# Performance work log

Measured on AMD Instinct MI355X. Metric: run time of the kernel, lower is better.

## Reference

```python
import jax, jax.numpy as jnp
import numpy as np
from jax import lax

N = 512          # batch size
A = 64 * 3 * 3 + 1  # 577 minibatch-disc input features
B = 32           # out_features of minibatch disc
C = 16           # kernel dimension


def leaky_relu(x, slope=0.2):
    return jnp.where(x >= 0, x, slope * x)


def setup_inputs() -> dict:
    key = jax.random.key(0)
    ks = jax.random.split(key, 9)
    readout = jax.random.normal(ks[0], (N, 1, 9, 9), dtype=jnp.float32)
    energy = jax.random.uniform(ks[1], (N,), dtype=jnp.float32)
    conv1_w = jax.random.normal(ks[2], (32, 1, 4, 4), dtype=jnp.float32) * 0.1
    conv2_w = jax.random.normal(ks[3], (64, 32, 4, 4), dtype=jnp.float32) * 0.05
    T = jax.random.normal(ks[4], (A, B * C), dtype=jnp.float32)  # init.normal(0,1)
    W1 = jax.random.normal(ks[5], (32, A + B), dtype=jnp.float32) * 0.04
    b1 = jax.random.normal(ks[6], (32,), dtype=jnp.float32) * 0.01
    W2 = jax.random.normal(ks[7], (1, 32), dtype=jnp.float32) * 0.1
    b2 = jax.random.normal(ks[8], (1,), dtype=jnp.float32) * 0.01
    return {"readout": readout, "energy": energy, "conv1_w": conv1_w,
            "conv2_w": conv2_w, "T": T, "W1": W1, "b1": b1, "W2": W2, "b2": b2}


def _conv(x, w):
    return lax.conv_general_dilated(
        x, w, window_strides=(1, 1), padding='VALID',
        dimension_numbers=('NCHW', 'OIHW', 'NCHW'))


def reference(readout, energy, conv1_w, conv2_w, T, W1, b1, W2, b2):
    n = readout.shape[0]
    # conv stack: (n,1,9,9) -> (n,32,6,6) -> (n,64,3,3)
    h = leaky_relu(_conv(readout, conv1_w))
    h = leaky_relu(_conv(h, conv2_w))
    hidden = h.reshape(n, -1)  # (n, 576)
    reco_energy = readout.reshape(n, -1).sum(axis=1)
    energy_diff = jnp.abs(reco_energy - energy)[:, None]  # (n,1)
    f = jnp.concatenate([hidden, energy_diff], axis=1)  # (n, 577)
    # minibatch discrimination
    M = (f @ T).reshape(n, B, C)                     # (n,B,C)
    # L1 pairwise distances, summed over kernel dim C: (n,n,B)
    L1 = jnp.abs(M[None, :, :, :] - M[:, None, :, :]).sum(axis=3)
    o = jnp.exp(-L1).sum(axis=0)                     # (n,B)
    x = jnp.concatenate([f, o], axis=1)              # (n, 609)
    x = leaky_relu(x @ W1.T + b1)
    x = jax.nn.sigmoid(x @ W2.T + b2)
    return x.squeeze()
```

## Files before the change

kernel.cpp:

```cpp
#include <hip/hip_runtime.h>

#define LRELU(v) ((v) >= 0.f ? (v) : 0.2f*(v))

#define ROROW(P, RB) \
    const float P##0=ro[(RB)+0], P##1=ro[(RB)+1], P##2=ro[(RB)+2], \
        P##3=ro[(RB)+3], P##4=ro[(RB)+4], P##5=ro[(RB)+5], \
        P##6=ro[(RB)+6], P##7=ro[(RB)+7], P##8=ro[(RB)+8];

#define C1X(X0,X1,X2,X3) \
    (wa.x*A##X0 + wa.y*A##X1 + wa.z*A##X2 + wa.w*A##X3 \
   + wb.x*B##X0 + wb.y*B##X1 + wb.z*B##X2 + wb.w*B##X3 \
   + wc.x*C##X0 + wc.y*C##X1 + wc.z*C##X2 + wc.w*C##X3 \
   + wd.x*D##X0 + wd.y*D##X1 + wd.z*D##X2 + wd.w*D##X3)

#define E0 q0.x
#define E1 q0.y
#define E2 q0.z
#define E3 q0.w
#define E4 q1.x
#define E5 q1.y
#define E6 q1.z
#define E7 q1.w
#define E8 q2.x
#define E9 q2.y
#define E10 q2.z
#define E11 q2.w
#define E12 q3.x
#define E13 q3.y
#define E14 q3.z
#define E15 q3.w
#define E16 q4.x
#define E17 q4.y
#define E18 q4.z
#define E19 q4.w
#define E20 q5.x
#define E21 q5.y
#define E22 q5.z
#define E23 q5.w
#define E24 q6.x
#define E25 q6.y
#define E26 q6.z
#define E27 q6.w
#define E28 q7.x
#define E29 q7.y
#define E30 q7.z
#define E31 q7.w
#define E32 q8.x
#define E33 q8.y
#define E34 q8.z
#define E35 q8.w

#define AT(P, A, B, C, D) a##P += w.x*E##A + w.y*E##B + w.z*E##C + w.w*E##D;

#define LD1(RK, K, BASE) { const int fidx_ = t + (K)*256; \
    const int woc_ = fidx_ >> 5, q4_ = fidx_ & 31; \
    RK = ((const float4*)w2)[(oc0 + woc_)*128 + (BASE) + q4_]; }
#define LDALL(BASE) LD1(r0,0,BASE) LD1(r1,1,BASE) LD1(r2,2,BASE) LD1(r3,3,BASE)
#define ST1(RK, K) { const int fidx_ = t + (K)*256; \
    const int woc_ = fidx_ >> 5, q4_ = fidx_ & 31; \
    *((float4*)&w2s[woc_*128 + ((q4_*4) ^ ((woc_ & 7) << 2))]) = RK; }
#define STALL ST1(r0,0) ST1(r1,1) ST1(r2,2) ST1(r3,3)

__global__ __launch_bounds__(256) void convf_kernel(
    const float* __restrict__ readout, const float* __restrict__ energy,
    const float* __restrict__ w1, const float* __restrict__ w2,
    const float* __restrict__ W1, float* __restrict__ f_ws,
    float* __restrict__ W1T)
{
    const int bid = blockIdx.x;
    const int n   = bid >> 1;
    const int och = bid & 1;
    const int oc0 = och << 5;
    const int t = threadIdx.x;
    __shared__ float ro[81];
    __shared__ float h1[1152];
    __shared__ float w2s[4096];
    __shared__ float red[2304];

    if (t < 81) ro[t] = readout[n*81 + t];
    __syncthreads();

    if (och == 0 && t < 64) {
        float v = ro[t];
        if (t < 17) v += ro[t + 64];
        #pragma unroll
        for (int m = 32; m; m >>= 1) v += __shfl_down(v, m);
        if (t == 0) f_ws[n*577 + 576] = fabsf(v - energy[n]);
    }

    if (t < 192) {
        const int oc1 = t & 31, y = t >> 5;
        const float4* wp4 = (const float4*)&w1[oc1*16];
        const float4 wa = wp4[0], wb = wp4[1], wc = wp4[2], wd = wp4[3];
        const int rb0 = y*9;
        ROROW(A, rb0)
        ROROW(B, rb0+9)
        ROROW(C, rb0+18)
        ROROW(D, rb0+27)
        float* hp = &h1[oc1*36 + y*6];
        float v;
        v = C1X(0,1,2,3); hp[0] = LRELU(v);
        v = C1X(1,2,3,4); hp[1] = LRELU(v);
        v = C1X(2,3,4,5); hp[2] = LRELU(v);
        v = C1X(3,4,5,6); hp[3] = LRELU(v);
        v = C1X(4,5,6,7); hp[4] = LRELU(v);
        v = C1X(5,6,7,8); hp[5] = LRELU(v);
    }

    float4 r0, r1, r2, r3;
    LDALL(0)
    __syncthreads();

    const int ich = t >> 5, ocl = t & 31;
    float a0=0.f,a1=0.f,a2=0.f,a3=0.f,a4=0.f,a5=0.f,a6=0.f,a7=0.f,a8=0.f;
    const int wbase = ocl*128;
    const int wswz  = (ocl & 7) << 2;

    for (int chunk = 0; chunk < 4; chunk++) {
        STALL
        __syncthreads();
        if (chunk < 3) { LDALL((chunk+1)*32) }
        {
            const int icw = ich;
            const int ic  = chunk*8 + ich;
            const float4* hp = (const float4*)&h1[ic*36];
            float4 q0=hp[0], q1=hp[1], q2=hp[2], q3=hp[3], q4=hp[4],
                   q5=hp[5], q6=hp[6], q7=hp[7], q8=hp[8];
            { float4 w = *((const float4*)&w2s[wbase + ((icw*16 + 0) ^ wswz)]);
              AT(0, 0,1,2,3)    AT(1, 1,2,3,4)    AT(2, 2,3,4,5)
              AT(3, 6,7,8,9)    AT(4, 7,8,9,10)   AT(5, 8,9,10,11)
              AT(6, 12,13,14,15) AT(7, 13,14,15,16) AT(8, 14,15,16,17) }
            { float4 w = *((const float4*)&w2s[wbase + ((icw*16 + 4) ^ wswz)]);
              AT(0, 6,7,8,9)    AT(1, 7,8,9,10)   AT(2, 8,9,10,11)
              AT(3, 12,13,14,15) AT(4, 13,14,15,16) AT(5, 14,15,16,17)
              AT(6, 18,19,20,21) AT(7, 19,20,21,22) AT(8, 20,21,22,23) }
            { float4 w = *((const float4*)&w2s[wbase + ((icw*16 + 8) ^ wswz)]);
              AT(0, 12,13,14,15) AT(1, 13,14,15,16) AT(2, 14,15,16,17)
              AT(3, 18,19,20,21) AT(4, 19,20,21,22) AT(5, 20,21,22,23)
              AT(6, 24,25,26,27) AT(7, 25,26,27,28) AT(8, 26,27,28,29) }
            { float4 w = *((const float4*)&w2s[wbase + ((icw*16 + 12) ^ wswz)]);
              AT(0, 18,19,20,21) AT(1, 19,20,21,22) AT(2, 20,21,22,23)
              AT(3, 24,25,26,27) AT(4, 25,26,27,28) AT(5, 26,27,28,29)
              AT(6, 30,31,32,33) AT(7, 31,32,33,34) AT(8, 32,33,34,35) }
        }
        __syncthreads();
    }

    {
        float* rp = &red[t*9];
        rp[0]=a0; rp[1]=a1; rp[2]=a2; rp[3]=a3; rp[4]=a4;
        rp[5]=a5; rp[6]=a6; rp[7]=a7; rp[8]=a8;
    }
    __syncthreads();
    for (int idx = t; idx < 288; idx += 256) {
        const int o2 = idx / 9, pos = idx % 9;
        float v = 0.f;
        #pragma unroll
        for (int k = 0; k < 8; k++) v += red[k*288 + idx];
        f_ws[n*577 + (oc0 + o2)*9 + pos] = LRELU(v);
    }

    if (bid < 8) {
        for (int idx = t; idx < 2436; idx += 256) {
            const int g = bid*2436 + idx;
            const int u = g & 31, a = g >> 5;
            W1T[g] = W1[u*609 + a];
        }
    }
}

__global__ __launch_bounds__(1024) void mgemm_kernel(
    const float* __restrict__ F, const float* __restrict__ T,
    float* __restrict__ M)
{
    const int t = threadIdx.x;
    const int rb = blockIdx.x >> 2;
    const int cb = blockIdx.x & 3;
    const int ws = __builtin_amdgcn_readfirstlane(t >> 6);
    const int lane = t & 63;
    const int c0 = cb*128 + lane*2;
    const int k0 = ws*36;
    const int k1 = (ws == 15) ? 577 : (k0 + 36);
    const int r0 = rb*8;
    __shared__ float red[8*1032];

    const float* fbase = F + r0*577;
    float x0=0.f,y0=0.f, x1=0.f,y1=0.f, x2=0.f,y2=0.f, x3=0.f,y3=0.f,
          x4=0.f,y4=0.f, x5=0.f,y5=0.f, x6=0.f,y6=0.f, x7=0.f,y7=0.f;
    #pragma unroll 4
    for (int k = k0; k < k1; ++k) {
        const float2 tv = *(const float2*)&T[k*512 + c0];
        const float* fr = fbase + k;
        const float f0v = fr[0],    f1v = fr[577],  f2v = fr[1154], f3v = fr[1731];
        const float f4v = fr[2308], f5v = fr[2885], f6v = fr[3462], f7v = fr[4039];
        x0 += f0v*tv.x; y0 += f0v*tv.y;
        x1 += f1v*tv.x; y1 += f1v*tv.y;
        x2 += f2v*tv.x; y2 += f2v*tv.y;
        x3 += f3v*tv.x; y3 += f3v*tv.y;
        x4 += f4v*tv.x; y4 += f4v*tv.y;
        x5 += f5v*tv.x; y5 += f5v*tv.y;
        x6 += f6v*tv.x; y6 += f6v*tv.y;
        x7 += f7v*tv.x; y7 += f7v*tv.y;
    }

    const int cl2 = lane*2;
    if (ws < 8) {
        float* rp = &red[ws*1032];
        *(float2*)&rp[0*128 + cl2] = make_float2(x0, y0);
        *(float2*)&rp[1*128 + cl2] = make_float2(x1, y1);
        *(float2*)&rp[2*128 + cl2] = make_float2(x2, y2);
        *(float2*)&rp[3*128 + cl2] = make_float2(x3, y3);
        *(float2*)&rp[4*128 + cl2] = make_float2(x4, y4);
        *(float2*)&rp[5*128 + cl2] = make_float2(x5, y5);
        *(float2*)&rp[6*128 + cl2] = make_float2(x6, y6);
        *(float2*)&rp[7*128 + cl2] = make_float2(x7, y7);
    }
    __syncthreads();
    if (ws >= 8) {
        float* rp = &red[(ws-8)*1032];
        float2 v;
        v = *(float2*)&rp[0*128 + cl2]; v.x += x0; v.y += y0; *(float2*)&rp[0*128 + cl2] = v;
        v = *(float2*)&rp[1*128 + cl2]; v.x += x1; v.y += y1; *(float2*)&rp[1*128 + cl2] = v;
        v = *(float2*)&rp[2*128 + cl2]; v.x += x2; v.y += y2; *(float2*)&rp[2*128 + cl2] = v;
        v = *(float2*)&rp[3*128 + cl2]; v.x += x3; v.y += y3; *(float2*)&rp[3*128 + cl2] = v;
        v = *(float2*)&rp[4*128 + cl2]; v.x += x4; v.y += y4; *(float2*)&rp[4*128 + cl2] = v;
        v = *(float2*)&rp[5*128 + cl2]; v.x += x5; v.y += y5; *(float2*)&rp[5*128 + cl2] = v;
        v = *(float2*)&rp[6*128 + cl2]; v.x += x6; v.y += y6; *(float2*)&rp[6*128 + cl2] = v;
        v = *(float2*)&rp[7*128 + cl2]; v.x += x7; v.y += y7; *(float2*)&rp[7*128 + cl2] = v;
    }
    __syncthreads();
    {
        const int row = t >> 7, col = t & 127;
        const int o = row*128 + col;
        float v = 0.f;
        #pragma unroll
        for (int p = 0; p < 8; p++) v += red[p*1032 + o];
        M[(r0 + row)*512 + cb*128 + col] = v;
    }
}

#define LDM(R0, R1, R2, R3, JOFF) { \
    const float4* p_ = (const float4*)&M[(j0+jl+(JOFF))*512 + b*16]; \
    R0 = p_[0]; R1 = p_[1]; R2 = p_[2]; R3 = p_[3]; }

#define S16(P0, P1, P2, P3) \
  (fabsf(v0.x-P0.x)+fabsf(v0.y-P0.y)+fabsf(v0.z-P0.z)+fabsf(v0.w-P0.w) \
  +fabsf(v1.x-P1.x)+fabsf(v1.y-P1.y)+fabsf(v1.z-P1.z)+fabsf(v1.w-P1.w) \
  +fabsf(v2.x-P2.x)+fabsf(v2.y-P2.y)+fabsf(v2.z-P2.z)+fabsf(v2.w-P2.w) \
  +fabsf(v3.x-P3.x)+fabsf(v3.y-P3.y)+fabsf(v3.z-P3.z)+fabsf(v3.w-P3.w))

__global__ __launch_bounds__(256) void pairwise_kernel(
    const float* __restrict__ M, float* __restrict__ o_part)
{
    const int jt  = blockIdx.x >> 5;
    const int isp = blockIdx.x & 31;
    const int t = threadIdx.x;
    const int b = t & 31, jl = t >> 5;
    const int j0 = jt * 32;
    __shared__ float mi[16*572];

    float4 mA0,mA1,mA2,mA3, mB0,mB1,mB2,mB3, mC0,mC1,mC2,mC3, mD0,mD1,mD2,mD3;
    LDM(mA0,mA1,mA2,mA3, 0)
    LDM(mB0,mB1,mB2,mB3, 8)
    LDM(mC0,mC1,mC2,mC3, 16)
    LDM(mD0,mD1,mD2,mD3, 24)

    const int i0 = isp * 16;
    #pragma unroll
    for (int k = 0; k < 8; k++) {
        const int q = k*256 + t;
        const int r = q >> 7;
        const int x = (q & 127) * 4;
        float4 v = *(const float4*)&M[(i0+r)*512 + x];
        *(float4*)&mi[r*572 + x + ((x>>5)<<2)] = v;
    }
    __syncthreads();

    float acc0 = 0.f, acc1 = 0.f, acc2 = 0.f, acc3 = 0.f;
    const int lbase = b*16 + ((b>>1)<<2);

    #pragma unroll 4
    for (int r = 0; r < 16; r++) {
        const float4* q_ = (const float4*)&mi[r*572 + lbase];
        const float4 v0 = q_[0], v1 = q_[1], v2 = q_[2], v3 = q_[3];
        acc0 += __expf(-(S16(mA0,mA1,mA2,mA3)));
        acc1 += __expf(-(S16(mB0,mB1,mB2,mB3)));
        acc2 += __expf(-(S16(mC0,mC1,mC2,mC3)));
        acc3 += __expf(-(S16(mD0,mD1,mD2,mD3)));
    }
    const int ob = isp*16384 + b;
    o_part[ob + (j0+jl   )*32] = acc0;
    o_part[ob + (j0+jl+8 )*32] = acc1;
    o_part[ob + (j0+jl+16)*32] = acc2;
    o_part[ob + (j0+jl+24)*32] = acc3;
}

__global__ __launch_bounds__(256) void mlp_kernel(
    const float* __restrict__ f, const float* __restrict__ o_part,
    const float* __restrict__ W1T, const float* __restrict__ b1v,
    const float* __restrict__ W2, const float* __restrict__ b2v,
    float* __restrict__ out)
{
    const int j = blockIdx.x;
    const int t = threadIdx.x;
    __shared__ float xs[609];
    __shared__ float red[256];

    for (int a = t; a < 577; a += 256) xs[a] = f[j*577 + a];
    {
        const int bb = t & 31, g = t >> 5;
        float ov = 0.f;
        #pragma unroll
        for (int k = 0; k < 4; k++)
            ov += o_part[(g + 8*k)*16384 + j*32 + bb];
        red[t] = ov;
    }
    __syncthreads();
    if (t < 32) {
        float ov = 0.f;
        #pragma unroll
        for (int g = 0; g < 8; g++) ov += red[t + g*32];
        xs[577 + t] = ov;
    }
    __syncthreads();

    const int u = t & 31, seg = t >> 5;
    float p = 0.f;
    #pragma unroll 4
    for (int a = seg; a < 609; a += 8)
        p += xs[a] * W1T[a*32 + u];
    red[t] = p;
    __syncthreads();

    if (t < 32) {
        float hid = red[t];
        #pragma unroll
        for (int s = 1; s < 8; s++) hid += red[t + s*32];
        hid += b1v[t];
        hid = LRELU(hid);
        float pr = hid * W2[t];
        #pragma unroll
        for (int mk = 16; mk; mk >>= 1) pr += __shfl_xor(pr, mk);
        if (t == 0) out[j] = 1.f / (1.f + __expf(-(pr + b2v[0])));
    }
}

extern "C" void kernel_launch(void* const* d_in, const int* in_sizes, int n_in,
                              void* d_out, int out_size, void* d_ws, size_t ws_size,
                              hipStream_t stream) {
    const float* readout = (const float*)d_in[0];
    const float* energy  = (const float*)d_in[1];
    const float* w1      = (const float*)d_in[2];
    const float* w2      = (const float*)d_in[3];
    const float* Tm      = (const float*)d_in[4];
    const float* W1      = (const float*)d_in[5];
    const float* b1v     = (const float*)d_in[6];
    const float* W2      = (const float*)d_in[7];
    const float* b2v     = (const float*)d_in[8];
    float* out = (float*)d_out;

    char* ws = (char*)d_ws;
    float* f_ws   = (float*)(ws);
    float* M_ws   = (float*)(ws + 512*577*4);
    float* o_ws   = (float*)(ws + 512*577*4 + 512*512*4);
    float* W1T_ws = (float*)(ws + 512*577*4 + 512*512*4 + 32*512*32*4);

    convf_kernel   <<<1024, 256, 0, stream>>>(readout, energy, w1, w2, W1, f_ws, W1T_ws);
    mgemm_kernel   <<<256, 1024, 0, stream>>>(f_ws, Tm, M_ws);
    pairwise_kernel<<<512, 256, 0, stream>>>(M_ws, o_ws);
    mlp_kernel     <<<512, 256, 0, stream>>>(f_ws, o_ws, W1T_ws, b1v, W2, b2v, out);
}
```

Baseline: 45.62 us.

## Restructure conv2 thread mapping with shuffle reduction and split pairwise i-range finer

The conv2 stage now gives each thread two output channels across 16 input-channel lanes. It loads weights in two larger chunks with a new swizzle and reduces partial sums with warp xor-shuffles, which drops the shared-memory reduction buffer and its extra barrier. The pairwise kernel splits the i dimension into 64 slices of 8 rows instead of 32 slices of 16, doubling the grid to raise parallelism. The mlp kernel sums 64 partials instead of 32 and the workspace offset is adjusted to match. The costs are higher register pressure and more partial-sum traffic.

```diff
diff --git a/kernel.cpp b/kernel.cpp
--- a/kernel.cpp
+++ b/kernel.cpp
@@ -50,16 +50,39 @@
 #define E34 q8.z
 #define E35 q8.w
 
-#define AT(P, A, B, C, D) a##P += w.x*E##A + w.y*E##B + w.z*E##C + w.w*E##D;
-
-#define LD1(RK, K, BASE) { const int fidx_ = t + (K)*256; \
-    const int woc_ = fidx_ >> 5, q4_ = fidx_ & 31; \
-    RK = ((const float4*)w2)[(oc0 + woc_)*128 + (BASE) + q4_]; }
-#define LDALL(BASE) LD1(r0,0,BASE) LD1(r1,1,BASE) LD1(r2,2,BASE) LD1(r3,3,BASE)
+#define AZ(P, I, A, B, C, D) P##I += w.x*E##A + w.y*E##B + w.z*E##C + w.w*E##D;
+
+#define KYB0(P) { AZ(P,0, 0,1,2,3)    AZ(P,1, 1,2,3,4)    AZ(P,2, 2,3,4,5) \
+                  AZ(P,3, 6,7,8,9)    AZ(P,4, 7,8,9,10)   AZ(P,5, 8,9,10,11) \
+                  AZ(P,6, 12,13,14,15) AZ(P,7, 13,14,15,16) AZ(P,8, 14,15,16,17) }
+#define KYB1(P) { AZ(P,0, 6,7,8,9)    AZ(P,1, 7,8,9,10)   AZ(P,2, 8,9,10,11) \
+                  AZ(P,3, 12,13,14,15) AZ(P,4, 13,14,15,16) AZ(P,5, 14,15,16,17) \
+                  AZ(P,6, 18,19,20,21) AZ(P,7, 19,20,21,22) AZ(P,8, 20,21,22,23) }
+#define KYB2(P) { AZ(P,0, 12,13,14,15) AZ(P,1, 13,14,15,16) AZ(P,2, 14,15,16,17) \
+                  AZ(P,3, 18,19,20,21) AZ(P,4, 19,20,21,22) AZ(P,5, 20,21,22,23) \
+                  AZ(P,6, 24,25,26,27) AZ(P,7, 25,26,27,28) AZ(P,8, 26,27,28,29) }
+#define KYB3(P) { AZ(P,0, 18,19,20,21) AZ(P,1, 19,20,21,22) AZ(P,2, 20,21,22,23) \
+                  AZ(P,3, 24,25,26,27) AZ(P,4, 25,26,27,28) AZ(P,5, 26,27,28,29) \
+                  AZ(P,6, 30,31,32,33) AZ(P,7, 31,32,33,34) AZ(P,8, 32,33,34,35) }
+
+#define RED18(M) \
+    a0+=__shfl_xor(a0,M); a1+=__shfl_xor(a1,M); a2+=__shfl_xor(a2,M); \
+    a3+=__shfl_xor(a3,M); a4+=__shfl_xor(a4,M); a5+=__shfl_xor(a5,M); \
+    a6+=__shfl_xor(a6,M); a7+=__shfl_xor(a7,M); a8+=__shfl_xor(a8,M); \
+    g0+=__shfl_xor(g0,M); g1+=__shfl_xor(g1,M); g2+=__shfl_xor(g2,M); \
+    g3+=__shfl_xor(g3,M); g4+=__shfl_xor(g4,M); g5+=__shfl_xor(g5,M); \
+    g6+=__shfl_xor(g6,M); g7+=__shfl_xor(g7,M); g8+=__shfl_xor(g8,M);
+
+#define LD1(RK, K, CH) { const int fidx_ = t + (K)*256; \
+    const int woc_ = fidx_ >> 6, q4_ = fidx_ & 63; \
+    RK = ((const float4*)w2)[(oc0 + woc_)*128 + (CH)*64 + q4_]; }
+#define LDALL(CH) LD1(r0,0,CH) LD1(r1,1,CH) LD1(r2,2,CH) LD1(r3,3,CH) \
+                  LD1(r4,4,CH) LD1(r5,5,CH) LD1(r6,6,CH) LD1(r7,7,CH)
 #define ST1(RK, K) { const int fidx_ = t + (K)*256; \
-    const int woc_ = fidx_ >> 5, q4_ = fidx_ & 31; \
-    *((float4*)&w2s[woc_*128 + ((q4_*4) ^ ((woc_ & 7) << 2))]) = RK; }
-#define STALL ST1(r0,0) ST1(r1,1) ST1(r2,2) ST1(r3,3)
+    const int woc_ = fidx_ >> 6, q4_ = fidx_ & 63; \
+    *((float4*)&w2s[woc_*256 + ((q4_*4) ^ (((woc_>>1)&3)<<3))]) = RK; }
+#define STALL ST1(r0,0) ST1(r1,1) ST1(r2,2) ST1(r3,3) \
+              ST1(r4,4) ST1(r5,5) ST1(r6,6) ST1(r7,7)
 
 __global__ __launch_bounds__(256) void convf_kernel(
     const float* __restrict__ readout, const float* __restrict__ energy,
@@ -74,8 +97,7 @@
     const int t = threadIdx.x;
     __shared__ float ro[81];
     __shared__ float h1[1152];
-    __shared__ float w2s[4096];
-    __shared__ float red[2304];
+    __shared__ float w2s[8192];
 
     if (t < 81) ro[t] = readout[n*81 + t];
     __syncthreads();
@@ -107,57 +129,51 @@
         v = C1X(5,6,7,8); hp[5] = LRELU(v);
     }
 
-    float4 r0, r1, r2, r3;
+    float4 r0, r1, r2, r3, r4, r5, r6, r7;
     LDALL(0)
     __syncthreads();
 
-    const int ich = t >> 5, ocl = t & 31;
+    const int ocp = t >> 4, ich = t & 15;
+    const int ocaL = ocp*2, ocbL = ocaL + 1;
+    const int wswz = (ocp & 3) << 3;
+    const int wbA = ocaL*256, wbB = ocbL*256;
     float a0=0.f,a1=0.f,a2=0.f,a3=0.f,a4=0.f,a5=0.f,a6=0.f,a7=0.f,a8=0.f;
-    const int wbase = ocl*128;
-    const int wswz  = (ocl & 7) << 2;
-
-    for (int chunk = 0; chunk < 4; chunk++) {
+    float g0=0.f,g1=0.f,g2=0.f,g3=0.f,g4=0.f,g5=0.f,g6=0.f,g7=0.f,g8=0.f;
+
+    #pragma unroll 1
+    for (int chunk = 0; chunk < 2; chunk++) {
         STALL
         __syncthreads();
-        if (chunk < 3) { LDALL((chunk+1)*32) }
-        {
-            const int icw = ich;
-            const int ic  = chunk*8 + ich;
-            const float4* hp = (const float4*)&h1[ic*36];
-            float4 q0=hp[0], q1=hp[1], q2=hp[2], q3=hp[3], q4=hp[4],
-                   q5=hp[5], q6=hp[6], q7=hp[7], q8=hp[8];
-            { float4 w = *((const float4*)&w2s[wbase + ((icw*16 + 0) ^ wswz)]);
-              AT(0, 0,1,2,3)    AT(1, 1,2,3,4)    AT(2, 2,3,4,5)
-              AT(3, 6,7,8,9)    AT(4, 7,8,9,10)   AT(5, 8,9,10,11)
-              AT(6, 12,13,14,15) AT(7, 13,14,15,16) AT(8, 14,15,16,17) }
-            { float4 w = *((const float4*)&w2s[wbase + ((icw*16 + 4) ^ wswz)]);
-              AT(0, 6,7,8,9)    AT(1, 7,8,9,10)   AT(2, 8,9,10,11)
-              AT(3, 12,13,14,15) AT(4, 13,14,15,16) AT(5, 14,15,16,17)
-              AT(6, 18,19,20,21) AT(7, 19,20,21,22) AT(8, 20,21,22,23) }
-            { float4 w = *((const float4*)&w2s[wbase + ((icw*16 + 8) ^ wswz)]);
-              AT(0, 12,13,14,15) AT(1, 13,14,15,16) AT(2, 14,15,16,17)
-              AT(3, 18,19,20,21) AT(4, 19,20,21,22) AT(5, 20,21,22,23)
-              AT(6, 24,25,26,27) AT(7, 25,26,27,28) AT(8, 26,27,28,29) }
-            { float4 w = *((const float4*)&w2s[wbase + ((icw*16 + 12) ^ wswz)]);
-              AT(0, 18,19,20,21) AT(1, 19,20,21,22) AT(2, 20,21,22,23)
-              AT(3, 24,25,26,27) AT(4, 25,26,27,28) AT(5, 26,27,28,29)
-              AT(6, 30,31,32,33) AT(7, 31,32,33,34) AT(8, 32,33,34,35) }
-        }
+        if (chunk == 0) { LDALL(1) }
+
+        const int ic = chunk*16 + ich;
+        const float4* hp = (const float4*)&h1[ic*36];
+        const float4 q0=hp[0], q1=hp[1], q2=hp[2], q3=hp[3], q4=hp[4],
+                     q5=hp[5], q6=hp[6], q7=hp[7], q8=hp[8];
+        const int colb = ich*16;
+        { float4 w = *((const float4*)&w2s[wbA + ((colb+ 0) ^ wswz)]); KYB0(a) }
+        { float4 w = *((const float4*)&w2s[wbA + ((colb+ 4) ^ wswz)]); KYB1(a) }
+        { float4 w = *((const float4*)&w2s[wbA + ((colb+ 8) ^ wswz)]); KYB2(a) }
+        { float4 w = *((const float4*)&w2s[wbA + ((colb+12) ^ wswz)]); KYB3(a) }
+        { float4 w = *((const float4*)&w2s[wbB + ((colb+ 0) ^ wswz)]); KYB0(g) }
+        { float4 w = *((const float4*)&w2s[wbB + ((colb+ 4) ^ wswz)]); KYB1(g) }
+        { float4 w = *((const float4*)&w2s[wbB + ((colb+ 8) ^ wswz)]); KYB2(g) }
+        { float4 w = *((const float4*)&w2s[wbB + ((colb+12) ^ wswz)]); KYB3(g) }
         __syncthreads();
     }
 
-    {
-        float* rp = &red[t*9];
-        rp[0]=a0; rp[1]=a1; rp[2]=a2; rp[3]=a3; rp[4]=a4;
-        rp[5]=a5; rp[6]=a6; rp[7]=a7; rp[8]=a8;
-    }
-    __syncthreads();
-    for (int idx = t; idx < 288; idx += 256) {
-        const int o2 = idx / 9, pos = idx % 9;
-        float v = 0.f;
-        #pragma unroll
-        for (int k = 0; k < 8; k++) v += red[k*288 + idx];
-        f_ws[n*577 + (oc0 + o2)*9 + pos] = LRELU(v);
+    RED18(1) RED18(2) RED18(4) RED18(8)
+
+    if (ich == 0) {
+        float* fa = &f_ws[n*577 + (oc0 + ocaL)*9];
+        float* fb = &f_ws[n*577 + (oc0 + ocbL)*9];
+        float v;
+        v=a0; fa[0]=LRELU(v); v=a1; fa[1]=LRELU(v); v=a2; fa[2]=LRELU(v);
+        v=a3; fa[3]=LRELU(v); v=a4; fa[4]=LRELU(v); v=a5; fa[5]=LRELU(v);
+        v=a6; fa[6]=LRELU(v); v=a7; fa[7]=LRELU(v); v=a8; fa[8]=LRELU(v);
+        v=g0; fb[0]=LRELU(v); v=g1; fb[1]=LRELU(v); v=g2; fb[2]=LRELU(v);
+        v=g3; fb[3]=LRELU(v); v=g4; fb[4]=LRELU(v); v=g5; fb[5]=LRELU(v);
+        v=g6; fb[6]=LRELU(v); v=g7; fb[7]=LRELU(v); v=g8; fb[8]=LRELU(v);
     }
 
     if (bid < 8) {
@@ -252,12 +268,12 @@
 __global__ __launch_bounds__(256) void pairwise_kernel(
     const float* __restrict__ M, float* __restrict__ o_part)
 {
-    const int jt  = blockIdx.x >> 5;
-    const int isp = blockIdx.x & 31;
+    const int jt  = blockIdx.x >> 6;
+    const int isp = blockIdx.x & 63;
     const int t = threadIdx.x;
     const int b = t & 31, jl = t >> 5;
     const int j0 = jt * 32;
-    __shared__ float mi[16*572];
+    __shared__ float mi[8*572];
 
     float4 mA0,mA1,mA2,mA3, mB0,mB1,mB2,mB3, mC0,mC1,mC2,mC3, mD0,mD1,mD2,mD3;
     LDM(mA0,mA1,mA2,mA3, 0)
@@ -265,9 +281,9 @@
     LDM(mC0,mC1,mC2,mC3, 16)
     LDM(mD0,mD1,mD2,mD3, 24)
 
-    const int i0 = isp * 16;
+    const int i0 = isp * 8;
     #pragma unroll
-    for (int k = 0; k < 8; k++) {
+    for (int k = 0; k < 4; k++) {
         const int q = k*256 + t;
         const int r = q >> 7;
         const int x = (q & 127) * 4;
@@ -279,8 +295,8 @@
     float acc0 = 0.f, acc1 = 0.f, acc2 = 0.f, acc3 = 0.f;
     const int lbase = b*16 + ((b>>1)<<2);
 
-    #pragma unroll 4
-    for (int r = 0; r < 16; r++) {
+    #pragma unroll
+    for (int r = 0; r < 8; r++) {
         const float4* q_ = (const float4*)&mi[r*572 + lbase];
         const float4 v0 = q_[0], v1 = q_[1], v2 = q_[2], v3 = q_[3];
         acc0 += __expf(-(S16(mA0,mA1,mA2,mA3)));
@@ -311,7 +327,7 @@
         const int bb = t & 31, g = t >> 5;
         float ov = 0.f;
         #pragma unroll
-        for (int k = 0; k < 4; k++)
+        for (int k = 0; k < 8; k++)
             ov += o_part[(g + 8*k)*16384 + j*32 + bb];
         red[t] = ov;
     }
@@ -363,10 +379,10 @@
     float* f_ws   = (float*)(ws);
     float* M_ws   = (float*)(ws + 512*577*4);
     float* o_ws   = (float*)(ws + 512*577*4 + 512*512*4);
-    float* W1T_ws = (float*)(ws + 512*577*4 + 512*512*4 + 32*512*32*4);
+    float* W1T_ws = (float*)(ws + 512*577*4 + 512*512*4 + 64*512*32*4);
 
     convf_kernel   <<<1024, 256, 0, stream>>>(readout, energy, w1, w2, W1, f_ws, W1T_ws);
     mgemm_kernel   <<<256, 1024, 0, stream>>>(f_ws, Tm, M_ws);
-    pairwise_kernel<<<512, 256, 0, stream>>>(M_ws, o_ws);
+    pairwise_kernel<<<1024, 256, 0, stream>>>(M_ws, o_ws);
     mlp_kernel     <<<512, 256, 0, stream>>>(f_ws, o_ws, W1T_ws, b1v, W2, b2v, out);
 }
```

After: 50.21 us. +10.0%, slower.
